# Performance work log

Measured on AMD Instinct MI355X. Metric: run time of the kernel, lower is better.

The kernel has to match this reference:

```python
import jax, jax.numpy as jnp
import numpy as np

B, T, C, H, W = 16, 5, 512, 16, 16
NUM_FEAT = 10
K_IN = T * H * W          # 1280, conv1/G3 in_channels
G_OUT = NUM_FEAT * H * W  # 2560, G3 out_channels


def setup_inputs() -> dict:
    key = jax.random.key(0)
    ks = jax.random.split(key, 9)
    inp = {
        "input": jax.random.normal(ks[0], (B, T, C, H, W), dtype=jnp.float32),
        "input1": jax.random.normal(ks[1], (B, T, C, H, W), dtype=jnp.float32),
        "act_weights": jax.random.uniform(ks[2], (3,), dtype=jnp.float32),
        # Conv1d kernels with kernel_size=1 stored as [out_ch, in_ch]
        "conv1_w": jax.random.normal(ks[3], (NUM_FEAT, K_IN), dtype=jnp.float32) / np.sqrt(K_IN),
        "conv1_b": jax.random.normal(ks[4], (NUM_FEAT,), dtype=jnp.float32) * 0.01,
        "G3_w": jax.random.normal(ks[5], (G_OUT, K_IN), dtype=jnp.float32) / np.sqrt(K_IN),
        "G3_b": jax.random.normal(ks[6], (G_OUT,), dtype=jnp.float32) * 0.01,
        "ffnn1_w": jax.random.normal(ks[7], (C, C), dtype=jnp.float32) / np.sqrt(C),
        "ffnn1_b": jax.random.normal(ks[8], (C,), dtype=jnp.float32) * 0.01,
    }
    return inp


def reference(input, input1, act_weights, conv1_w, conv1_b, G3_w, G3_b, ffnn1_w, ffnn1_b):
    b, t, c, h, w = input.shape
    nf = conv1_w.shape[0]
    # [B,T,C,H,W] -> [B,C,T*H*W] -> transpose to [B, T*H*W, C] (conv1d channel axis = T*H*W)
    x = jnp.transpose(input, (0, 2, 1, 3, 4)).reshape(b, c, t * h * w)
    x = jnp.swapaxes(x, 1, 2)  # [B, K_IN, C]

    # conv1 (1x1 conv == GEMM over channel axis): [B, nf, C]
    c1 = jnp.einsum("fk,bkc->bfc", conv1_w, x) + conv1_b[None, :, None]
    # transpose -> [B, C, nf]; AvgPool1d(nf) -> mean over nf -> [B, C]
    pooled = jnp.mean(jnp.swapaxes(c1, 1, 2), axis=-1)
    # shared linear (same ffnn1 used in all three branches)
    pre = pooled @ ffnn1_w.T + ffnn1_b  # [B, C]

    # G3: [B, G_OUT, C] -> permute -> [B, C, G_OUT]
    g3 = jnp.einsum("gk,bkc->bgc", G3_w, x) + G3_b[None, :, None]
    g3 = jnp.swapaxes(g3, 1, 2)  # [B, C, G_OUT]

    # diag_embed(v) @ M == v[..., None] * M  -> fuse the three branches into one scale
    scale = (act_weights[0] * jax.nn.relu(pre)
             + act_weights[1] * jax.nn.sigmoid(pre)
             + act_weights[2] * jax.nn.softmax(pre, axis=1))  # [B, C]

    out = scale[:, :, None] * g3  # [B, C, nf*H*W]
    out = out.reshape(b, c, nf, h, w)
    return jnp.transpose(out, (0, 2, 1, 3, 4))  # [B, nf, C, H, W]
```

## Files before the change

kernel.cpp:

```cpp
#include <hip/hip_runtime.h>
#include <hip/hip_bf16.h>
#include <stdint.h>

#define B_   16
#define T_   5
#define C_   512
#define HW_  256
#define NF_  10
#define KIN_ 1280
#define GOUT_ 2560

typedef __attribute__((ext_vector_type(8))) short s16x8;
typedef __attribute__((ext_vector_type(4))) float f32x4;
typedef unsigned short u16;

__device__ __forceinline__ u16 f2bf(float x) {
    unsigned int u = __float_as_uint(x);
    return (u16)((u + 0x7FFFu + ((u >> 16) & 1u)) >> 16);
}

#define CASTW_N8  (GOUT_ * KIN_ / 8)
#define CASTW_BLKS (CASTW_N8 / 256)

__global__ __launch_bounds__(256) void k_init(const float* __restrict__ conv1_w,
                        const float* __restrict__ conv1_b,
                        float* __restrict__ wbar, float* __restrict__ bbar,
                        const float* __restrict__ g3w,
                        u16* __restrict__ wsA) {
    if (blockIdx.x < 5) {
        int k = blockIdx.x * 256 + threadIdx.x;
        float s = 0.f;
        #pragma unroll
        for (int f = 0; f < NF_; ++f) s += conv1_w[f * KIN_ + k];
        wbar[k] = s * (1.0f / NF_);
        if (blockIdx.x == 0 && threadIdx.x == 0) {
            float sb = 0.f;
            #pragma unroll
            for (int f = 0; f < NF_; ++f) sb += conv1_b[f];
            *bbar = sb * (1.0f / NF_);
        }
        return;
    }
    int i = (blockIdx.x - 5) * 256 + threadIdx.x;
    if (i < CASTW_N8) {
        const float4* s = reinterpret_cast<const float4*>(g3w) + (size_t)i * 2;
        float4 v0 = s[0], v1 = s[1];
        union { u16 h[8]; int4 v; } u;
        u.h[0] = f2bf(v0.x); u.h[1] = f2bf(v0.y); u.h[2] = f2bf(v0.z); u.h[3] = f2bf(v0.w);
        u.h[4] = f2bf(v1.x); u.h[5] = f2bf(v1.y); u.h[6] = f2bf(v1.z); u.h[7] = f2bf(v1.w);
        reinterpret_cast<int4*>(wsA)[i] = u.v;
    }
}

__global__ void k_wbar(const float* __restrict__ conv1_w,
                       const float* __restrict__ conv1_b,
                       float* __restrict__ wbar, float* __restrict__ bbar) {
    int k = blockIdx.x * blockDim.x + threadIdx.x;
    if (k < KIN_) {
        float s = 0.f;
        #pragma unroll
        for (int f = 0; f < NF_; ++f) s += conv1_w[f * KIN_ + k];
        wbar[k] = s * (1.0f / NF_);
    }
    if (blockIdx.x == 0 && threadIdx.x == 0) {
        float s = 0.f;
        #pragma unroll
        for (int f = 0; f < NF_; ++f) s += conv1_b[f];
        *bbar = s * (1.0f / NF_);
    }
}

#define FUSE_BLKS (B_ * C_)

__global__ __launch_bounds__(256) void k_prep(const float* __restrict__ in,
                         const float* __restrict__ wbar,
                         const float* __restrict__ bbar,
                         float* __restrict__ pooled,
                         u16* __restrict__ X) {
    int bc = blockIdx.x;
    int b = bc >> 9;
    int c = bc & 511;
    int tid = threadIdx.x;

    float s = 0.f;
    if (tid < 160) {
        int t   = tid >> 5;
        int hw0 = (tid & 31) * 8;
        size_t off = ((size_t)(b * T_ + t) * C_ + c) * HW_ + hw0;
        const float4* ip = reinterpret_cast<const float4*>(in + off);
        float4 v0 = ip[0], v1 = ip[1];
        const float4* wp = reinterpret_cast<const float4*>(wbar + t * HW_ + hw0);
        float4 w0 = wp[0], w1 = wp[1];
        s = v0.x * w0.x + v0.y * w0.y + v0.z * w0.z + v0.w * w0.w
          + v1.x * w1.x + v1.y * w1.y + v1.z * w1.z + v1.w * w1.w;
        union { u16 h[8]; int4 q; } u;
        u.h[0] = f2bf(v0.x); u.h[1] = f2bf(v0.y); u.h[2] = f2bf(v0.z); u.h[3] = f2bf(v0.w);
        u.h[4] = f2bf(v1.x); u.h[5] = f2bf(v1.y); u.h[6] = f2bf(v1.z); u.h[7] = f2bf(v1.w);
        reinterpret_cast<int4*>(X + off)[0] = u.q;
    }

    #pragma unroll
    for (int off = 32; off > 0; off >>= 1) s += __shfl_down(s, off, 64);
    __shared__ float red[4];
    int wid = tid >> 6, lane = tid & 63;
    if (lane == 0) red[wid] = s;
    __syncthreads();
    if (tid == 0) {
        float tot = red[0] + red[1] + red[2] + red[3];
        pooled[bc] = tot + *bbar;
    }
}

__global__ __launch_bounds__(256) void k_pooled(const float* __restrict__ in,
                         const float* __restrict__ wbar,
                         const float* __restrict__ bbar,
                         float* __restrict__ pooled) {
    int bc = blockIdx.x;
    int b = bc >> 9;
    int c = bc & 511;
    int hw = threadIdx.x;
    const float* base = in + ((size_t)(b * T_) * C_ + c) * HW_;
    float s = 0.f;
    #pragma unroll
    for (int t = 0; t < T_; ++t)
        s = fmaf(wbar[t * HW_ + hw], base[(size_t)t * C_ * HW_ + hw], s);
    #pragma unroll
    for (int off = 32; off > 0; off >>= 1) s += __shfl_down(s, off, 64);
    __shared__ float red[4];
    int wid = threadIdx.x >> 6, lane = threadIdx.x & 63;
    if (lane == 0) red[wid] = s;
    __syncthreads();
    if (threadIdx.x == 0) {
        float tot = red[0] + red[1] + red[2] + red[3];
        pooled[bc] = tot + *bbar;
    }
}

__global__ __launch_bounds__(256) void k_pre(const float* __restrict__ pooled,
                       const float* __restrict__ ffnn1_w,
                       const float* __restrict__ ffnn1_b,
                       float* __restrict__ pre) {
    int b   = blockIdx.x >> 4;
    int grp = blockIdx.x & 15;
    int wid = threadIdx.x >> 6, lane = threadIdx.x & 63;

    const float4* pp = reinterpret_cast<const float4*>(pooled + b * C_ + lane * 8);
    float4 pa = pp[0], pb = pp[1];

    #pragma unroll
    for (int rr = 0; rr < 8; ++rr) {
        int c = grp * 32 + wid * 8 + rr;
        const float4* wr = reinterpret_cast<const float4*>(ffnn1_w + (size_t)c * C_ + lane * 8);
        float4 wa = wr[0], wb2 = wr[1];
        float d = pa.x * wa.x + pa.y * wa.y + pa.z * wa.z + pa.w * wa.w
                + pb.x * wb2.x + pb.y * wb2.y + pb.z * wb2.z + pb.w * wb2.w;
        #pragma unroll
        for (int off = 32; off > 0; off >>= 1) d += __shfl_xor(d, off, 64);
        if (lane == 0) pre[b * C_ + c] = d + ffnn1_b[c];
    }
}

__global__ __launch_bounds__(512) void k_scale(const float* __restrict__ pooled,
                        const float* __restrict__ ffnn1_w,
                        const float* __restrict__ ffnn1_b,
                        const float* __restrict__ actw,
                        float* __restrict__ scale) {
    int b = blockIdx.x;
    int c = threadIdx.x;
    __shared__ float sp[C_];
    __shared__ float red[8];

    sp[c] = pooled[b * C_ + c];
    __syncthreads();

    float acc = ffnn1_b[c];
    const float* wr = ffnn1_w + (size_t)c * C_;
    #pragma unroll 8
    for (int j = 0; j < C_; ++j) acc = fmaf(wr[j], sp[j], acc);

    int wid = c >> 6, lane = c & 63;
    float m = acc;
    #pragma unroll
    for (int off = 32; off > 0; off >>= 1) m = fmaxf(m, __shfl_down(m, off, 64));
    if (lane == 0) red[wid] = m;
    __syncthreads();
    if (c == 0) {
        float mm = red[0];
        #pragma unroll
        for (int i = 1; i < 8; ++i) mm = fmaxf(mm, red[i]);
        red[0] = mm;
    }
    __syncthreads();
    m = red[0];
    __syncthreads();

    float e = __expf(acc - m);
    float s = e;
    #pragma unroll
    for (int off = 32; off > 0; off >>= 1) s += __shfl_down(s, off, 64);
    if (lane == 0) red[wid] = s;
    __syncthreads();
    if (c == 0) {
        float ss = 0.f;
        #pragma unroll
        for (int i = 0; i < 8; ++i) ss += red[i];
        red[0] = ss;
    }
    __syncthreads();
    s = red[0];

    float w0 = actw[0], w1 = actw[1], w2 = actw[2];
    float val = w0 * fmaxf(acc, 0.f)
              + w1 * (1.f / (1.f + __expf(-acc)))
              + w2 * (e / s);
    scale[b * C_ + c] = val;
}

#define BM 160
#define BN 256
#define BK 32
#define NKT (KIN_ / BK)
#define ABUF (BM * BK)
#define BBUF (BN * BK)
#define BUFU (ABUF + BBUF)

__device__ __forceinline__ void gload16(const void* g, void* l) {
    __builtin_amdgcn_global_load_lds(
        (const __attribute__((address_space(1))) void*)g,
        (__attribute__((address_space(3))) void*)l, 16, 0, 0);
}

__global__ __launch_bounds__(256, 2) void k_gemm_mfma(
    const u16* __restrict__ A,
    const u16* __restrict__ X,
    const float* __restrict__ g3b,
    const float* __restrict__ pre,
    const float* __restrict__ actw,
    float* __restrict__ out)
{
    __shared__ u16 lds[2 * BUFU];
    __shared__ float sS[BN];
    __shared__ float redm[4], reds[4];

    int orig = blockIdx.x;
    int xcd  = orig & 7;
    int idx  = orig >> 3;
    int nt   = xcd * 4 + (idx >> 4);
    int gt   = idx & 15;
    int g0   = gt * BM;
    int b    = nt >> 1;
    int c0   = (nt & 1) * BN;

    int tid = threadIdx.x;
    int lane = tid & 63, wid = tid >> 6;
    int lrow = lane & 15, lslot = lane >> 4;

    int offA0, offA1, offA2, offB0, offB1, offB2, offB3;
    {
        int q, r, p;
        q = tid;        r = q >> 2; p = q & 3; offA0 = r * KIN_ + (p ^ ((r >> 1) & 3)) * 8;
        q = 256 + tid;  r = q >> 2; p = q & 3; offA1 = r * KIN_ + (p ^ ((r >> 1) & 3)) * 8;
        q = 512 + tid;  r = q >> 2; p = q & 3; offA2 = r * KIN_ + (p ^ ((r >> 1) & 3)) * 8;
        q = tid;        r = q >> 2; p = q & 3; offB0 = r * HW_  + (p ^ ((r >> 1) & 3)) * 8;
        q = 256 + tid;  r = q >> 2; p = q & 3; offB1 = r * HW_  + (p ^ ((r >> 1) & 3)) * 8;
        q = 512 + tid;  r = q >> 2; p = q & 3; offB2 = r * HW_  + (p ^ ((r >> 1) & 3)) * 8;
        q = 768 + tid;  r = q >> 2; p = q & 3; offB3 = r * HW_  + (p ^ ((r >> 1) & 3)) * 8;
    }
    int wb = wid * 512;

    const u16* Abase = A + (size_t)g0 * KIN_;
    #define XOFF(kt) ((((size_t)(b * T_ + ((kt) >> 3)) * C_) + c0) * HW_ + ((kt) & 7) * 32)

    #define STAGE(D, sA, sX)                                                 \
    {                                                                        \
        gload16((sA) + offA0, (D) + wb);                                     \
        gload16((sA) + offA1, (D) + 2048 + wb);                              \
        if (tid < 128) gload16((sA) + offA2, (D) + 4096 + wb);               \
        gload16((sX) + offB0, (D) + ABUF + wb);                              \
        gload16((sX) + offB1, (D) + ABUF + 2048 + wb);                       \
        gload16((sX) + offB2, (D) + ABUF + 4096 + wb);                       \
        gload16((sX) + offB3, (D) + ABUF + 6144 + wb);                       \
    }

    float p0 = pre[b * C_ + tid];
    float p1 = pre[b * C_ + 256 + tid];
    float aw0 = actw[0], aw1 = actw[1], aw2 = actw[2];

    STAGE(lds, Abase, X + XOFF(0));

    float mx = fmaxf(p0, p1);
    #pragma unroll
    for (int off = 32; off > 0; off >>= 1) mx = fmaxf(mx, __shfl_xor(mx, off, 64));
    if (lane == 0) redm[wid] = mx;
    __syncthreads();
    float m = fmaxf(fmaxf(redm[0], redm[1]), fmaxf(redm[2], redm[3]));
    float e0 = __expf(p0 - m), e1 = __expf(p1 - m);
    float sm = e0 + e1;
    #pragma unroll
    for (int off = 32; off > 0; off >>= 1) sm += __shfl_xor(sm, off, 64);
    if (lane == 0) reds[wid] = sm;
    __syncthreads();
    float ssum = reds[0] + reds[1] + reds[2] + reds[3];
    {
        float pc = (c0 == 0) ? p0 : p1;
        float ec = (c0 == 0) ? e0 : e1;
        sS[tid] = aw0 * fmaxf(pc, 0.f)
                + aw1 * (1.f / (1.f + __expf(-pc)))
                + aw2 * (ec / ssum);
    }

    f32x4 acc[10][4];
    #pragma unroll
    for (int mI = 0; mI < 10; ++mI)
        #pragma unroll
        for (int n = 0; n < 4; ++n) acc[mI][n] = (f32x4)0.f;

    int cur = 0;
    for (int t = 0; t < NKT; ++t) {
        const u16* Ac = lds + cur * BUFU;
        const u16* Bc = Ac + ABUF;
        if (t + 1 < NKT) {
            u16* Dn = lds + (cur ^ 1) * BUFU;
            const u16* sA = Abase + (size_t)(t + 1) * BK;
            const u16* sX = X + XOFF(t + 1);
            STAGE(Dn, sA, sX);
        }

        s16x8 b0[4];
        #pragma unroll
        for (int n = 0; n < 4; ++n) {
            int r = wid * 64 + n * 16 + lrow;
            int p = lslot ^ ((r >> 1) & 3);
            b0[n] = *reinterpret_cast<const s16x8*>(Bc + r * BK + p * 8);
        }
        __builtin_amdgcn_s_setprio(1);
        #pragma unroll
        for (int mI = 0; mI < 10; ++mI) {
            int r = mI * 16 + lrow;
            int p = lslot ^ ((r >> 1) & 3);
            s16x8 am = *reinterpret_cast<const s16x8*>(Ac + r * BK + p * 8);
            #pragma unroll
            for (int n = 0; n < 4; ++n)
                acc[mI][n] = __builtin_amdgcn_mfma_f32_16x16x32_bf16(
                                am, b0[n], acc[mI][n], 0, 0, 0);
        }
        __builtin_amdgcn_s_setprio(0);

        __syncthreads();
        cur ^= 1;
    }

    #pragma unroll
    for (int n = 0; n < 4; ++n) {
        int cl = wid * 64 + n * 16 + lrow;
        int c  = c0 + cl;
        float sc = sS[cl];
        #pragma unroll
        for (int mI = 0; mI < 10; ++mI) {
            int g  = g0 + mI * 16 + lslot * 4;
            int f  = g >> 8;
            int hw = g & 255;
            float4 bias = *reinterpret_cast<const float4*>(g3b + g);
            f32x4 v = acc[mI][n];
            float4 o;
            o.x = sc * (v[0] + bias.x);
            o.y = sc * (v[1] + bias.y);
            o.z = sc * (v[2] + bias.z);
            o.w = sc * (v[3] + bias.w);
            *reinterpret_cast<float4*>(
                out + (((size_t)(b * NF_ + f) * C_ + c) * HW_ + hw)) = o;
        }
    }
    #undef XOFF
    #undef STAGE
}

#define FBM 128
#define FBN 128
#define FBK 32
__global__ __launch_bounds__(256) void k_gemm_fp32(
    const float* __restrict__ in,
    const float* __restrict__ g3w,
    const float* __restrict__ g3b,
    const float* __restrict__ scale,
    float* __restrict__ out)
{
    int b  = blockIdx.y;
    int gt = blockIdx.x >> 2;
    int ct = blockIdx.x & 3;
    int g0 = gt * FBM, c0 = ct * FBN;
    int tid = threadIdx.x;
    int ty = tid & 15;
    int tx = tid >> 4;

    __shared__ float As[FBK][FBM + 4];
    __shared__ float Bs[FBK][FBN + 4];

    float acc[8][8];
    #pragma unroll
    for (int i = 0; i < 8; ++i)
        #pragma unroll
        for (int j = 0; j < 8; ++j) acc[i][j] = 0.f;

    for (int k0 = 0; k0 < KIN_; k0 += FBK) {
        int t   = k0 >> 8;
        int hw0 = k0 & 255;
        #pragma unroll
        for (int p = 0; p < 16; ++p) {
            int idx = tid + p * 256;
            int kk = idx & 31, gg = idx >> 5;
            As[kk][gg] = g3w[(size_t)(g0 + gg) * KIN_ + k0 + kk];
        }
        const float* bsrc = in + ((size_t)(b * T_ + t) * C_ + c0) * HW_ + hw0;
        #pragma unroll
        for (int p = 0; p < 16; ++p) {
            int idx = tid + p * 256;
            int kk = idx & 31, cc = idx >> 5;
            Bs[kk][cc] = bsrc[(size_t)cc * HW_ + kk];
        }
        __syncthreads();
        #pragma unroll
        for (int kk = 0; kk < FBK; ++kk) {
            float a[8], bb[8];
            #pragma unroll
            for (int i = 0; i < 8; ++i) a[i] = As[kk][ty * 8 + i];
            #pragma unroll
            for (int j = 0; j < 8; ++j) bb[j] = Bs[kk][tx * 8 + j];
            #pragma unroll
            for (int i = 0; i < 8; ++i)
                #pragma unroll
                for (int j = 0; j < 8; ++j)
                    acc[i][j] = fmaf(a[i], bb[j], acc[i][j]);
        }
        __syncthreads();
    }

    int gl = ty * 8;
    int g  = g0 + gl;
    int f  = g >> 8;
    int hw = g & 255;
    #pragma unroll
    for (int j = 0; j < 8; ++j) {
        int c = c0 + tx * 8 + j;
        float sc = scale[b * C_ + c];
        float* op = out + (((size_t)(b * NF_ + f) * C_ + c) * HW_ + hw);
        float4 v0, v1;
        v0.x = sc * (acc[0][j] + g3b[g + 0]);
        v0.y = sc * (acc[1][j] + g3b[g + 1]);
        v0.z = sc * (acc[2][j] + g3b[g + 2]);
        v0.w = sc * (acc[3][j] + g3b[g + 3]);
        v1.x = sc * (acc[4][j] + g3b[g + 4]);
        v1.y = sc * (acc[5][j] + g3b[g + 5]);
        v1.z = sc * (acc[6][j] + g3b[g + 6]);
        v1.w = sc * (acc[7][j] + g3b[g + 7]);
        reinterpret_cast<float4*>(op)[0] = v0;
        reinterpret_cast<float4*>(op)[1] = v1;
    }
}

extern "C" void kernel_launch(void* const* d_in, const int* in_sizes, int n_in,
                              void* d_out, int out_size, void* d_ws, size_t ws_size,
                              hipStream_t stream) {
    const float* input    = (const float*)d_in[0];
    const float* actw     = (const float*)d_in[2];
    const float* conv1_w  = (const float*)d_in[3];
    const float* conv1_b  = (const float*)d_in[4];
    const float* g3w      = (const float*)d_in[5];
    const float* g3b      = (const float*)d_in[6];
    const float* ffnn1_w  = (const float*)d_in[7];
    const float* ffnn1_b  = (const float*)d_in[8];
    float* out = (float*)d_out;

    float* ws     = (float*)d_ws;
    float* wbar   = ws;
    float* bbar   = ws + KIN_;
    float* pooled = ws + 1536;
    float* pre    = ws + 1536 + B_ * C_;
    u16* wsA = (u16*)(ws + 17920);
    u16* wsX = wsA + (size_t)GOUT_ * KIN_;
    const size_t need = 71680ull + (size_t)GOUT_ * KIN_ * 2 + (size_t)B_ * T_ * C_ * HW_ * 2;

    if (ws_size >= need) {
        k_init<<<dim3(5 + CASTW_BLKS), dim3(256), 0, stream>>>(
            conv1_w, conv1_b, wbar, bbar, g3w, wsA);
        k_prep<<<dim3(FUSE_BLKS), dim3(256), 0, stream>>>(
            input, wbar, bbar, pooled, wsX);
        k_pre<<<dim3(256), dim3(256), 0, stream>>>(pooled, ffnn1_w, ffnn1_b, pre);
        k_gemm_mfma<<<dim3(512), dim3(256), 0, stream>>>(
            wsA, wsX, g3b, pre, actw, out);
    } else {
        k_wbar<<<dim3((KIN_ + 255) / 256), dim3(256), 0, stream>>>(conv1_w, conv1_b, wbar, bbar);
        k_pooled<<<dim3(B_ * C_), dim3(256), 0, stream>>>(input, wbar, bbar, pooled);
        k_scale<<<dim3(B_), dim3(512), 0, stream>>>(pooled, ffnn1_w, ffnn1_b, actw, pre);
        k_gemm_fp32<<<dim3((GOUT_ / FBM) * (C_ / FBN), B_), dim3(256), 0, stream>>>(
            input, g3w, g3b, pre, out);
    }
}
```

Baseline: 89.90 us.

## Enlarge MFMA GEMM tile to 320x256 with 8 waves and triple-buffered LDS

Doubles the GEMM block tile along G to 320 rows using 512-thread blocks laid out as a 2x4 wave grid, halving the grid to 256 blocks. It replaces double buffering with a three-stage LDS ring that prefetches two K-steps ahead. Each prefetch is split into two halves interleaved with the two MFMA halves, using explicit vmcnt/lgkmcnt waits and raw barriers. The aim is to get more reuse per LDS load and to hide global-load latency. The cost is one block per CU, higher register and LDS pressure, and fragile hand-tuned wait counts.

Result: no change. 88.20 us (-1.9%).

```diff
diff --git a/kernel.cpp b/kernel.cpp
--- a/kernel.cpp
+++ b/kernel.cpp
@@ -216,7 +216,7 @@
     scale[b * C_ + c] = val;
 }
 
-#define BM 160
+#define BM 320
 #define BN 256
 #define BK 32
 #define NKT (KIN_ / BK)
@@ -230,7 +230,7 @@
         (__attribute__((address_space(3))) void*)l, 16, 0, 0);
 }
 
-__global__ __launch_bounds__(256, 2) void k_gemm_mfma(
+__global__ __launch_bounds__(512, 1) void k_gemm_mfma(
     const u16* __restrict__ A,
     const u16* __restrict__ X,
     const float* __restrict__ g3b,
@@ -238,76 +238,83 @@
     const float* __restrict__ actw,
     float* __restrict__ out)
 {
-    __shared__ u16 lds[2 * BUFU];
+    __shared__ u16 lds[3 * BUFU];
     __shared__ float sS[BN];
-    __shared__ float redm[4], reds[4];
+    __shared__ float redm[8], reds[8];
 
     int orig = blockIdx.x;
     int xcd  = orig & 7;
     int idx  = orig >> 3;
-    int nt   = xcd * 4 + (idx >> 4);
-    int gt   = idx & 15;
+    int nt   = xcd * 4 + (idx >> 3);
+    int gt   = idx & 7;
     int g0   = gt * BM;
     int b    = nt >> 1;
     int c0   = (nt & 1) * BN;
 
     int tid = threadIdx.x;
     int lane = tid & 63, wid = tid >> 6;
+    int wr = wid >> 2, wc = wid & 3;
     int lrow = lane & 15, lslot = lane >> 4;
 
-    int offA0, offA1, offA2, offB0, offB1, offB2, offB3;
+    int offA0, offA1, offA2, offB0, offB1;
     {
         int q, r, p;
-        q = tid;        r = q >> 2; p = q & 3; offA0 = r * KIN_ + (p ^ ((r >> 1) & 3)) * 8;
-        q = 256 + tid;  r = q >> 2; p = q & 3; offA1 = r * KIN_ + (p ^ ((r >> 1) & 3)) * 8;
-        q = 512 + tid;  r = q >> 2; p = q & 3; offA2 = r * KIN_ + (p ^ ((r >> 1) & 3)) * 8;
-        q = tid;        r = q >> 2; p = q & 3; offB0 = r * HW_  + (p ^ ((r >> 1) & 3)) * 8;
-        q = 256 + tid;  r = q >> 2; p = q & 3; offB1 = r * HW_  + (p ^ ((r >> 1) & 3)) * 8;
-        q = 512 + tid;  r = q >> 2; p = q & 3; offB2 = r * HW_  + (p ^ ((r >> 1) & 3)) * 8;
-        q = 768 + tid;  r = q >> 2; p = q & 3; offB3 = r * HW_  + (p ^ ((r >> 1) & 3)) * 8;
+        q = tid;         r = q >> 2; p = q & 3; offA0 = r * KIN_ + (p ^ ((r >> 1) & 3)) * 8;
+        q = 512 + tid;   r = q >> 2; p = q & 3; offA1 = r * KIN_ + (p ^ ((r >> 1) & 3)) * 8;
+        q = 1024 + tid;  r = q >> 2; p = q & 3; offA2 = r * KIN_ + (p ^ ((r >> 1) & 3)) * 8;
+        q = tid;         r = q >> 2; p = q & 3; offB0 = r * HW_  + (p ^ ((r >> 1) & 3)) * 8;
+        q = 512 + tid;   r = q >> 2; p = q & 3; offB1 = r * HW_  + (p ^ ((r >> 1) & 3)) * 8;
     }
     int wb = wid * 512;
 
     const u16* Abase = A + (size_t)g0 * KIN_;
     #define XOFF(kt) ((((size_t)(b * T_ + ((kt) >> 3)) * C_) + c0) * HW_ + ((kt) & 7) * 32)
 
-    #define STAGE(D, sA, sX)                                                 \
+    #define STAGE_H1(D, sA, sX)                                              \
     {                                                                        \
         gload16((sA) + offA0, (D) + wb);                                     \
-        gload16((sA) + offA1, (D) + 2048 + wb);                              \
-        if (tid < 128) gload16((sA) + offA2, (D) + 4096 + wb);               \
+        gload16((sA) + offA1, (D) + 4096 + wb);                              \
         gload16((sX) + offB0, (D) + ABUF + wb);                              \
-        gload16((sX) + offB1, (D) + ABUF + 2048 + wb);                       \
-        gload16((sX) + offB2, (D) + ABUF + 4096 + wb);                       \
-        gload16((sX) + offB3, (D) + ABUF + 6144 + wb);                       \
-    }
-
-    float p0 = pre[b * C_ + tid];
-    float p1 = pre[b * C_ + 256 + tid];
-    float aw0 = actw[0], aw1 = actw[1], aw2 = actw[2];
-
-    STAGE(lds, Abase, X + XOFF(0));
-
-    float mx = fmaxf(p0, p1);
-    #pragma unroll
-    for (int off = 32; off > 0; off >>= 1) mx = fmaxf(mx, __shfl_xor(mx, off, 64));
-    if (lane == 0) redm[wid] = mx;
-    __syncthreads();
-    float m = fmaxf(fmaxf(redm[0], redm[1]), fmaxf(redm[2], redm[3]));
-    float e0 = __expf(p0 - m), e1 = __expf(p1 - m);
-    float sm = e0 + e1;
-    #pragma unroll
-    for (int off = 32; off > 0; off >>= 1) sm += __shfl_xor(sm, off, 64);
-    if (lane == 0) reds[wid] = sm;
-    __syncthreads();
-    float ssum = reds[0] + reds[1] + reds[2] + reds[3];
+    }
+    #define STAGE_H2(D, sA, sX)                                              \
+    {                                                                        \
+        if (tid < 256) gload16((sA) + offA2, (D) + 8192 + wb);               \
+        gload16((sX) + offB1, (D) + ABUF + 4096 + wb);                       \
+    }
+
     {
-        float pc = (c0 == 0) ? p0 : p1;
-        float ec = (c0 == 0) ? e0 : e1;
-        sS[tid] = aw0 * fmaxf(pc, 0.f)
-                + aw1 * (1.f / (1.f + __expf(-pc)))
-                + aw2 * (ec / ssum);
-    }
+        float p0 = pre[b * C_ + tid];
+        float aw0 = actw[0], aw1 = actw[1], aw2 = actw[2];
+        float mx = p0;
+        #pragma unroll
+        for (int off = 32; off > 0; off >>= 1) mx = fmaxf(mx, __shfl_xor(mx, off, 64));
+        if (lane == 0) redm[wid] = mx;
+        __syncthreads();
+        float m8 = redm[0];
+        #pragma unroll
+        for (int i = 1; i < 8; ++i) m8 = fmaxf(m8, redm[i]);
+        float e0 = __expf(p0 - m8);
+        float sm = e0;
+        #pragma unroll
+        for (int off = 32; off > 0; off >>= 1) sm += __shfl_xor(sm, off, 64);
+        if (lane == 0) reds[wid] = sm;
+        __syncthreads();
+        float ssum = reds[0];
+        #pragma unroll
+        for (int i = 1; i < 8; ++i) ssum += reds[i];
+        if ((tid >> 8) == (c0 >> 8))
+            sS[tid & 255] = aw0 * fmaxf(p0, 0.f)
+                          + aw1 * (1.f / (1.f + __expf(-p0)))
+                          + aw2 * (e0 / ssum);
+    }
+
+    STAGE_H1(lds, Abase, X + XOFF(0));
+    STAGE_H2(lds, Abase, X + XOFF(0));
+    STAGE_H1(lds + BUFU, Abase + BK, X + XOFF(1));
+    STAGE_H2(lds + BUFU, Abase + BK, X + XOFF(1));
+    if (tid < 256) asm volatile("s_waitcnt vmcnt(5)" ::: "memory");
+    else           asm volatile("s_waitcnt vmcnt(4)" ::: "memory");
+    __builtin_amdgcn_s_barrier();
 
     f32x4 acc[10][4];
     #pragma unroll
@@ -319,45 +326,76 @@
     for (int t = 0; t < NKT; ++t) {
         const u16* Ac = lds + cur * BUFU;
         const u16* Bc = Ac + ABUF;
-        if (t + 1 < NKT) {
-            u16* Dn = lds + (cur ^ 1) * BUFU;
-            const u16* sA = Abase + (size_t)(t + 1) * BK;
-            const u16* sX = X + XOFF(t + 1);
-            STAGE(Dn, sA, sX);
-        }
-
-        s16x8 b0[4];
+        bool pre2 = (t + 2) < NKT;
+        int nx = cur + 2; if (nx >= 3) nx -= 3;
+        u16* Dn = lds + nx * BUFU;
+        const u16* sA = Abase + (size_t)(t + 2) * BK;
+        const u16* sX = X + XOFF(pre2 ? (t + 2) : 0);
+
+        s16x8 b0[4], a0[5];
         #pragma unroll
         for (int n = 0; n < 4; ++n) {
-            int r = wid * 64 + n * 16 + lrow;
+            int r = wc * 64 + n * 16 + lrow;
             int p = lslot ^ ((r >> 1) & 3);
             b0[n] = *reinterpret_cast<const s16x8*>(Bc + r * BK + p * 8);
         }
+        #pragma unroll
+        for (int mI = 0; mI < 5; ++mI) {
+            int r = wr * 160 + mI * 16 + lrow;
+            int p = lslot ^ ((r >> 1) & 3);
+            a0[mI] = *reinterpret_cast<const s16x8*>(Ac + r * BK + p * 8);
+        }
+        if (pre2) STAGE_H1(Dn, sA, sX);
+        __builtin_amdgcn_s_barrier();
+        asm volatile("s_waitcnt lgkmcnt(0)" ::: "memory");
+        __builtin_amdgcn_sched_barrier(0);
         __builtin_amdgcn_s_setprio(1);
         #pragma unroll
-        for (int mI = 0; mI < 10; ++mI) {
-            int r = mI * 16 + lrow;
-            int p = lslot ^ ((r >> 1) & 3);
-            s16x8 am = *reinterpret_cast<const s16x8*>(Ac + r * BK + p * 8);
+        for (int mI = 0; mI < 5; ++mI)
             #pragma unroll
             for (int n = 0; n < 4; ++n)
                 acc[mI][n] = __builtin_amdgcn_mfma_f32_16x16x32_bf16(
-                                am, b0[n], acc[mI][n], 0, 0, 0);
-        }
+                                a0[mI], b0[n], acc[mI][n], 0, 0, 0);
         __builtin_amdgcn_s_setprio(0);
 
-        __syncthreads();
-        cur ^= 1;
+        s16x8 a1[5];
+        #pragma unroll
+        for (int mI = 0; mI < 5; ++mI) {
+            int r = wr * 160 + (mI + 5) * 16 + lrow;
+            int p = lslot ^ ((r >> 1) & 3);
+            a1[mI] = *reinterpret_cast<const s16x8*>(Ac + r * BK + p * 8);
+        }
+        if (pre2) STAGE_H2(Dn, sA, sX);
+        __builtin_amdgcn_s_barrier();
+        asm volatile("s_waitcnt lgkmcnt(0)" ::: "memory");
+        __builtin_amdgcn_sched_barrier(0);
+        __builtin_amdgcn_s_setprio(1);
+        #pragma unroll
+        for (int mI = 0; mI < 5; ++mI)
+            #pragma unroll
+            for (int n = 0; n < 4; ++n)
+                acc[mI + 5][n] = __builtin_amdgcn_mfma_f32_16x16x32_bf16(
+                                    a1[mI], b0[n], acc[mI + 5][n], 0, 0, 0);
+        __builtin_amdgcn_s_setprio(0);
+
+        if (pre2) {
+            if (tid < 256) asm volatile("s_waitcnt vmcnt(5)" ::: "memory");
+            else           asm volatile("s_waitcnt vmcnt(4)" ::: "memory");
+        } else {
+            asm volatile("s_waitcnt vmcnt(0)" ::: "memory");
+        }
+        __builtin_amdgcn_s_barrier();
+        ++cur; if (cur >= 3) cur -= 3;
     }
 
     #pragma unroll
     for (int n = 0; n < 4; ++n) {
-        int cl = wid * 64 + n * 16 + lrow;
+        int cl = wc * 64 + n * 16 + lrow;
         int c  = c0 + cl;
         float sc = sS[cl];
         #pragma unroll
         for (int mI = 0; mI < 10; ++mI) {
-            int g  = g0 + mI * 16 + lslot * 4;
+            int g  = g0 + wr * 160 + mI * 16 + lslot * 4;
             int f  = g >> 8;
             int hw = g & 255;
             float4 bias = *reinterpret_cast<const float4*>(g3b + g);
@@ -372,7 +410,8 @@
         }
     }
     #undef XOFF
-    #undef STAGE
+    #undef STAGE_H1
+    #undef STAGE_H2
 }
 
 #define FBM 128
@@ -486,7 +525,7 @@
         k_prep<<<dim3(FUSE_BLKS), dim3(256), 0, stream>>>(
             input, wbar, bbar, pooled, wsX);
         k_pre<<<dim3(256), dim3(256), 0, stream>>>(pooled, ffnn1_w, ffnn1_b, pre);
-        k_gemm_mfma<<<dim3(512), dim3(256), 0, stream>>>(
+        k_gemm_mfma<<<dim3(256), dim3(512), 0, stream>>>(
             wsA, wsX, g3b, pre, actw, out);
     } else {
         k_wbar<<<dim3((KIN_ + 255) / 256), dim3(256), 0, stream>>>(conv1_w, conv1_b, wbar, bbar);
```
